# Optimization experiments

Hardware: AMD Instinct MI355X
Metric: run time of the kernel (lower is better)

The kernel has to match this reference:

```python
import jax, jax.numpy as jnp
import numpy as np

B = 16      # number of point clouds
N = 4096    # points per cloud (max after densify)
D = 3       # xyz


def setup_inputs() -> dict:
    key = jax.random.key(0)
    k1, k2 = jax.random.split(key)
    pred = jax.random.normal(k1, (B * N, D), dtype=jnp.float32)
    target = jax.random.normal(k2, (B * N, D), dtype=jnp.float32)
    # sorted segment ids, equal-sized clouds (faithful to to_dense_batch usage)
    batch = jnp.repeat(jnp.arange(B, dtype=jnp.int64), N)
    return {"pred": pred, "target": target, "batch": batch}


def to_dense_batch(x, batch, num_batches, max_n):
    # PyG to_dense_batch: scatter flat points into [B, max_n, D], zero-padded.
    ones = jnp.ones_like(batch)
    counts = jax.ops.segment_sum(ones, batch, num_segments=num_batches)
    offsets = jnp.concatenate([jnp.zeros((1,), batch.dtype), jnp.cumsum(counts)[:-1]])
    pos = jnp.arange(batch.shape[0], dtype=batch.dtype) - offsets[batch]
    dense = jnp.zeros((num_batches, max_n, x.shape[-1]), x.dtype)
    return dense.at[batch, pos].set(x)


def chamfer_distance(x, y):
    # squared-euclidean pairwise distances via the GEMM identity
    x2 = jnp.sum(x * x, axis=-1)                      # [B, N]
    y2 = jnp.sum(y * y, axis=-1)                      # [B, M]
    xy = jnp.einsum('bnd,bmd->bnm', x, y)             # [B, N, M]
    d = x2[:, :, None] + y2[:, None, :] - 2.0 * xy    # [B, N, M]
    cham_x = jnp.mean(jnp.min(d, axis=2), axis=1)     # mean over N of min over M
    cham_y = jnp.mean(jnp.min(d, axis=1), axis=1)     # mean over M of min over N
    # point_reduction='mean', batch_reduction='mean' (pytorch3d defaults)
    return jnp.mean(cham_x + cham_y)


def reference(pred, target, batch):
    x = to_dense_batch(pred, batch, B, N)
    y = to_dense_batch(target, batch, B, N)
    return chamfer_distance(x, y)
```

## Files before the change

### kernel.cpp

```cpp
#include <hip/hip_runtime.h>


namespace {

constexpr int kB = 16;
constexpr int kN = 4096;
constexpr int kPlane = kB * kN;
constexpr int kJS = 8;
constexpr int kJSL = kN / kJS;
constexpr float kScale = 1.0f / (float)(kB * kN);

typedef short bf16x8 __attribute__((ext_vector_type(8)));
typedef float f32x16 __attribute__((ext_vector_type(16)));
typedef unsigned short u16;

__device__ inline u16 bf16_rn(float f) {
  union { float f; unsigned u; } v; v.f = f;
  unsigned r = v.u + 0x7fffu + ((v.u >> 16) & 1u);
  return (u16)(r >> 16);
}
__device__ inline float bf16_f(u16 h) {
  union { unsigned u; float f; } v; v.u = (unsigned)h << 16;
  return v.f;
}
__device__ inline unsigned pk2(u16 lo, u16 hi) {
  return (unsigned)lo | ((unsigned)hi << 16);
}

__device__ inline float min3f(float a, float b, float c) {
  float d;
  asm("v_min3_f32 %0, %1, %2, %3" : "=v"(d) : "v"(a), "v"(b), "v"(c));
  return d;
}

__global__ void init_out(float* out) { out[0] = 0.0f; }

__global__ __launch_bounds__(256) void cd_mfma(
    const float* __restrict__ pred, const float* __restrict__ targ,
    float* __restrict__ colpart, float* __restrict__ rowpart,
    float* __restrict__ out) {
  __shared__ uint4 Blds4[kJSL * 2];
  __shared__ float clds[4 * kJSL];

  const int t = threadIdx.x;
  const int w = t >> 6, lane = t & 63;
  const int half = lane >> 5, l31 = lane & 31;
  const int chunk = blockIdx.x;
  const int cloud = blockIdx.y;
  const int slice = blockIdx.z;

  if ((t | chunk | cloud | slice) == 0) out[0] = 0.0f;

  const u16 one = 0x3F80;

  const int arow = cloud * kN + chunk * 128 + w * 32 + l31;
  union { uint4 u; bf16x8 v; } afu;
  {
    const float a = pred[3 * arow], c = pred[3 * arow + 1], d = pred[3 * arow + 2];
    const u16 ah = bf16_rn(a), ch = bf16_rn(c), dh = bf16_rn(d);
    const u16 al = bf16_rn(a - bf16_f(ah));
    const u16 cl = bf16_rn(c - bf16_f(ch));
    const u16 dl = bf16_rn(d - bf16_f(dh));
    const float s2 = fmaf(a, a, fmaf(c, c, d * d));
    const u16 s2h = bf16_rn(s2);
    const u16 s2l = bf16_rn(s2 - bf16_f(s2h));
    if (half == 0) {
      afu.u.x = pk2(ah, ch); afu.u.y = pk2(dh, al);
      afu.u.z = pk2(cl, dl); afu.u.w = pk2(ah, ch);
    } else {
      afu.u.x = pk2(dh, s2h); afu.u.y = pk2(s2l, one);
      afu.u.z = pk2(one, al); afu.u.w = pk2(cl, dl);
    }
  }
  const bf16x8 afrag = afu.v;

  {
    const float* tb = targ + (size_t)(cloud * kN + slice * kJSL) * 3;
    char* bl = (char*)Blds4;
    for (int pl = t; pl < kJSL; pl += 256) {
      const float a = tb[3 * pl], c = tb[3 * pl + 1], d = tb[3 * pl + 2];
      const u16 ah0 = bf16_rn(a), ch0 = bf16_rn(c), dh0 = bf16_rn(d);
      const u16 ah = bf16_rn(-2.0f * bf16_f(ah0));
      const u16 ch = bf16_rn(-2.0f * bf16_f(ch0));
      const u16 dh = bf16_rn(-2.0f * bf16_f(dh0));
      const u16 al = bf16_rn(-2.0f * bf16_f(bf16_rn(a - bf16_f(ah0))));
      const u16 cl = bf16_rn(-2.0f * bf16_f(bf16_rn(c - bf16_f(ch0))));
      const u16 dl = bf16_rn(-2.0f * bf16_f(bf16_rn(d - bf16_f(dh0))));
      const float s2 = fmaf(a, a, fmaf(c, c, d * d));
      const u16 s2h = bf16_rn(s2);
      const u16 s2l = bf16_rn(s2 - bf16_f(s2h));
      uint4 w0, w1;
      w0.x = pk2(ah, ch); w0.y = pk2(dh, ah); w0.z = pk2(ch, dh); w0.w = pk2(al, cl);
      w1.x = pk2(dl, one); w1.y = pk2(one, s2h); w1.z = pk2(s2l, al); w1.w = pk2(cl, dl);
      const int sw = (pl & 7) << 4;
      *reinterpret_cast<uint4*>(bl + ((pl * 32) ^ sw)) = w0;
      *reinterpret_cast<uint4*>(bl + ((pl * 32 + 16) ^ sw)) = w1;
    }
  }
  __syncthreads();

  f32x16 zacc;
#pragma unroll
  for (int r = 0; r < 16; ++r) zacc[r] = 0.0f;
  float rmin[16];
#pragma unroll
  for (int r = 0; r < 16; ++r) rmin[r] = 1e30f;

  constexpr int NT = kJSL / 64;
  const char* bl = (const char*)Blds4;
  int addr0 = (l31 * 32 + half * 16) ^ ((l31 & 7) << 4);
  for (int jt = 0; jt < NT; ++jt) {
    union { uint4 u; bf16x8 v; } B0, B1;
    B0.u = *reinterpret_cast<const uint4*>(bl + addr0);
    B1.u = *reinterpret_cast<const uint4*>(bl + addr0 + 1024);
    addr0 += 2048;
    const f32x16 s0 = __builtin_amdgcn_mfma_f32_32x32x16_bf16(afrag, B0.v, zacc, 0, 0, 0);
    const f32x16 s1 = __builtin_amdgcn_mfma_f32_32x32x16_bf16(afrag, B1.v, zacc, 0, 0, 0);
    float a0 = min3f(s0[0], s0[1], s0[2]);
    float a1 = min3f(s0[3], s0[4], s0[5]);
    float a2 = min3f(s0[6], s0[7], s0[8]);
    float a3 = min3f(s0[9], s0[10], s0[11]);
    float a4 = min3f(s0[12], s0[13], s0[14]);
    float cm0 = fminf(min3f(a0, a1, a2), min3f(a3, a4, s0[15]));
    float b0t = min3f(s1[0], s1[1], s1[2]);
    float b1t = min3f(s1[3], s1[4], s1[5]);
    float b2t = min3f(s1[6], s1[7], s1[8]);
    float b3t = min3f(s1[9], s1[10], s1[11]);
    float b4t = min3f(s1[12], s1[13], s1[14]);
    float cm1 = fminf(min3f(b0t, b1t, b2t), min3f(b3t, b4t, s1[15]));
#pragma unroll
    for (int r = 0; r < 16; ++r)
      asm("v_min3_f32 %0, %0, %1, %2" : "+v"(rmin[r]) : "v"(s0[r]), "v"(s1[r]));
    cm0 = fminf(cm0, __shfl_xor(cm0, 32, 64));
    cm1 = fminf(cm1, __shfl_xor(cm1, 32, 64));
    if (half == 0) {
      clds[w * kJSL + jt * 64 + l31] = cm0;
      clds[w * kJSL + jt * 64 + 32 + l31] = cm1;
    }
  }

#pragma unroll
  for (int st = 1; st < 32; st <<= 1) {
#pragma unroll
    for (int r = 0; r < 16; ++r)
      rmin[r] = fminf(rmin[r], __shfl_xor(rmin[r], st, 64));
  }
  if (l31 == 0) {
    float* rp = rowpart + ((size_t)slice * kB + cloud) * kN + chunk * 128 + w * 32;
#pragma unroll
    for (int r = 0; r < 16; ++r) {
      const int row = (r & 3) + 8 * (r >> 2) + 4 * half;
      rp[row] = rmin[r];
    }
  }

  __syncthreads();
  for (int j = t; j < kJSL; j += 256) {
    const float m = fminf(fminf(clds[j], clds[kJSL + j]),
                          fminf(clds[2 * kJSL + j], clds[3 * kJSL + j]));
    colpart[((size_t)cloud * 32 + chunk) * kN + slice * kJSL + j] = m;
  }
}

__global__ __launch_bounds__(256) void cd_reduce(
    const float* __restrict__ colpart, const float* __restrict__ rowpart,
    float* __restrict__ out) {
  const int u = blockIdx.x * 256 + threadIdx.x;
  const int cloud = u >> 12, p = u & (kN - 1);
  float rm = 1e30f;
#pragma unroll
  for (int s2 = 0; s2 < kJS; ++s2)
    rm = fminf(rm, rowpart[((size_t)s2 * kB + cloud) * kN + p]);
  const float* cp = colpart + (size_t)cloud * 32 * kN + p;
  float cm = 1e30f;
#pragma unroll 8
  for (int c = 0; c < 32; ++c) cm = fminf(cm, cp[(size_t)c * kN]);
  float s = rm + cm;
  for (int o = 32; o > 0; o >>= 1) s += __shfl_down(s, o, 64);
  __shared__ float wsum[4];
  const int lane = threadIdx.x & 63, wv = threadIdx.x >> 6;
  if (lane == 0) wsum[wv] = s;
  __syncthreads();
  if (threadIdx.x == 0)
    atomicAdd(out, (wsum[0] + wsum[1] + wsum[2] + wsum[3]) * kScale);
}

template <int KX>
__global__ __launch_bounds__(256) void chamfer_direct(
    const float* __restrict__ pred, const float* __restrict__ targ,
    float* __restrict__ out) {
  __shared__ float4 tA[128], tB[128];
  const int t = threadIdx.x;
  const int xb = blockIdx.x, b = blockIdx.y, dir = blockIdx.z;
  const float* __restrict__ X = dir ? targ : pred;
  const float* __restrict__ Y = dir ? pred : targ;
  float2 xx2[KX], xy2[KX], xz2[KX];
  float x2[KX], mn[KX];
  const int ibase = b * kN + xb * (256 * KX) + t;
#pragma unroll
  for (int k = 0; k < KX; ++k) {
    const int i = ibase + k * 256;
    const float a = X[3 * i], c = X[3 * i + 1], d = X[3 * i + 2];
    x2[k] = fmaf(a, a, fmaf(c, c, d * d));
    xx2[k] = make_float2(-2.0f * a, -2.0f * a);
    xy2[k] = make_float2(-2.0f * c, -2.0f * c);
    xz2[k] = make_float2(-2.0f * d, -2.0f * d);
    mn[k] = 1e30f;
  }
  for (int t0 = 0; t0 < kN; t0 += 256) {
    __syncthreads();
    if (t < 128) {
      const int j0 = 3 * (b * kN + t0 + 2 * t);
      const float a0 = Y[j0], c0 = Y[j0 + 1], d0 = Y[j0 + 2];
      const float a1 = Y[j0 + 3], c1 = Y[j0 + 4], d1 = Y[j0 + 5];
      tA[t] = make_float4(a0, a1, c0, c1);
      tB[t] = make_float4(d0, d1, fmaf(a0, a0, fmaf(c0, c0, d0 * d0)),
                          fmaf(a1, a1, fmaf(c1, c1, d1 * d1)));
    }
    __syncthreads();
    for (int jj = 0; jj < 128; ++jj) {
      const float4 qa = tA[jj], qb = tB[jj];
      const float2 qx = make_float2(qa.x, qa.y), qy = make_float2(qa.z, qa.w);
      const float2 qz = make_float2(qb.x, qb.y), qw = make_float2(qb.z, qb.w);
#pragma unroll
      for (int k = 0; k < KX; ++k) {
        float2 acc;
        asm("v_pk_fma_f32 %0, %1, %2, %3\n\t"
            "v_pk_fma_f32 %0, %4, %5, %0\n\t"
            "v_pk_fma_f32 %0, %6, %7, %0"
            : "=&v"(acc)
            : "v"(xz2[k]), "v"(qz), "v"(qw), "v"(xy2[k]), "v"(qy),
              "v"(xx2[k]), "v"(qx));
        asm("v_min3_f32 %0, %0, %1, %2" : "+v"(mn[k]) : "v"(acc.x), "v"(acc.y));
      }
    }
  }
  float s = 0.0f;
#pragma unroll
  for (int k = 0; k < KX; ++k) s += x2[k] + mn[k];
  for (int o = 32; o > 0; o >>= 1) s += __shfl_down(s, o, 64);
  __shared__ float wsum[4];
  const int lane = t & 63, wv = t >> 6;
  if (lane == 0) wsum[wv] = s;
  __syncthreads();
  if (t == 0)
    atomicAdd(out, (wsum[0] + wsum[1] + wsum[2] + wsum[3]) * kScale);
}

}

extern "C" void kernel_launch(void* const* d_in, const int* in_sizes, int n_in,
                              void* d_out, int out_size, void* d_ws,
                              size_t ws_size, hipStream_t stream) {
  const float* pred = (const float*)d_in[0];
  const float* targ = (const float*)d_in[1];
  float* out = (float*)d_out;

  const size_t needCol = (size_t)kB * 32 * kN * sizeof(float);
  const size_t needRow = (size_t)kJS * kPlane * sizeof(float);
  if (ws_size >= needCol + needRow) {
    float* colpart = (float*)d_ws;
    float* rowpart = (float*)((char*)d_ws + needCol);
    cd_mfma<<<dim3(32, kB, kJS), 256, 0, stream>>>(pred, targ, colpart,
                                                   rowpart, out);
    cd_reduce<<<dim3(kPlane / 256), 256, 0, stream>>>(colpart, rowpart, out);
  } else {
    init_out<<<dim3(1), dim3(1), 0, stream>>>(out);
    constexpr int KX = 8;
    dim3 grid(kN / (256 * KX), kB, 2);
    chamfer_direct<KX><<<grid, 256, 0, stream>>>(pred, targ, out);
  }
}
```

Measured before the change: 100.8 us.

## Fuse chamfer into one MFMA kernel computing both directions with row mins

The previous design computed the distance matrix once and extracted both row minima and column minima. Column minima were written to workspace partial buffers, and a second reduce kernel combined them. The new design runs the MFMA distance computation twice, once per direction (grid z=2). Each block streams the full other cloud through shared memory in 512-point stages and keeps only per-row minima reduced in registers, finishing with an atomic add. This removes the column-min shuffles and LDS writes, the workspace traffic and the reduce launch, but doubles MFMA work and adds per-stage syncs.

New measurement: 94.53 us. 6.2% less time.

```diff
diff --git a/kernel.cpp b/kernel.cpp
--- a/kernel.cpp
+++ b/kernel.cpp
@@ -5,9 +5,8 @@
 
 constexpr int kB = 16;
 constexpr int kN = 4096;
-constexpr int kPlane = kB * kN;
-constexpr int kJS = 8;
-constexpr int kJSL = kN / kJS;
+constexpr int kStage = 512;
+constexpr int kNS = kN / kStage;
 constexpr float kScale = 1.0f / (float)(kB * kN);
 
 typedef short bf16x8 __attribute__((ext_vector_type(8)));
@@ -27,36 +26,29 @@
   return (unsigned)lo | ((unsigned)hi << 16);
 }
 
-__device__ inline float min3f(float a, float b, float c) {
-  float d;
-  asm("v_min3_f32 %0, %1, %2, %3" : "=v"(d) : "v"(a), "v"(b), "v"(c));
-  return d;
-}
-
 __global__ void init_out(float* out) { out[0] = 0.0f; }
 
-__global__ __launch_bounds__(256) void cd_mfma(
+__global__ __launch_bounds__(256) void cd_fused(
     const float* __restrict__ pred, const float* __restrict__ targ,
-    float* __restrict__ colpart, float* __restrict__ rowpart,
     float* __restrict__ out) {
-  __shared__ uint4 Blds4[kJSL * 2];
-  __shared__ float clds[4 * kJSL];
+  __shared__ uint4 Blds4[kStage * 2];
+  __shared__ float wsum[4];
 
   const int t = threadIdx.x;
   const int w = t >> 6, lane = t & 63;
   const int half = lane >> 5, l31 = lane & 31;
   const int chunk = blockIdx.x;
   const int cloud = blockIdx.y;
-  const int slice = blockIdx.z;
-
-  if ((t | chunk | cloud | slice) == 0) out[0] = 0.0f;
+  const int dir = blockIdx.z;
+  const float* __restrict__ X = dir ? targ : pred;
+  const float* __restrict__ Y = dir ? pred : targ;
 
   const u16 one = 0x3F80;
 
   const int arow = cloud * kN + chunk * 128 + w * 32 + l31;
   union { uint4 u; bf16x8 v; } afu;
   {
-    const float a = pred[3 * arow], c = pred[3 * arow + 1], d = pred[3 * arow + 2];
+    const float a = X[3 * arow], c = X[3 * arow + 1], d = X[3 * arow + 2];
     const u16 ah = bf16_rn(a), ch = bf16_rn(c), dh = bf16_rn(d);
     const u16 al = bf16_rn(a - bf16_f(ah));
     const u16 cl = bf16_rn(c - bf16_f(ch));
@@ -74,31 +66,6 @@
   }
   const bf16x8 afrag = afu.v;
 
-  {
-    const float* tb = targ + (size_t)(cloud * kN + slice * kJSL) * 3;
-    char* bl = (char*)Blds4;
-    for (int pl = t; pl < kJSL; pl += 256) {
-      const float a = tb[3 * pl], c = tb[3 * pl + 1], d = tb[3 * pl + 2];
-      const u16 ah0 = bf16_rn(a), ch0 = bf16_rn(c), dh0 = bf16_rn(d);
-      const u16 ah = bf16_rn(-2.0f * bf16_f(ah0));
-      const u16 ch = bf16_rn(-2.0f * bf16_f(ch0));
-      const u16 dh = bf16_rn(-2.0f * bf16_f(dh0));
-      const u16 al = bf16_rn(-2.0f * bf16_f(bf16_rn(a - bf16_f(ah0))));
-      const u16 cl = bf16_rn(-2.0f * bf16_f(bf16_rn(c - bf16_f(ch0))));
-      const u16 dl = bf16_rn(-2.0f * bf16_f(bf16_rn(d - bf16_f(dh0))));
-      const float s2 = fmaf(a, a, fmaf(c, c, d * d));
-      const u16 s2h = bf16_rn(s2);
-      const u16 s2l = bf16_rn(s2 - bf16_f(s2h));
-      uint4 w0, w1;
-      w0.x = pk2(ah, ch); w0.y = pk2(dh, ah); w0.z = pk2(ch, dh); w0.w = pk2(al, cl);
-      w1.x = pk2(dl, one); w1.y = pk2(one, s2h); w1.z = pk2(s2l, al); w1.w = pk2(cl, dl);
-      const int sw = (pl & 7) << 4;
-      *reinterpret_cast<uint4*>(bl + ((pl * 32) ^ sw)) = w0;
-      *reinterpret_cast<uint4*>(bl + ((pl * 32 + 16) ^ sw)) = w1;
-    }
-  }
-  __syncthreads();
-
   f32x16 zacc;
 #pragma unroll
   for (int r = 0; r < 16; ++r) zacc[r] = 0.0f;
@@ -106,36 +73,54 @@
 #pragma unroll
   for (int r = 0; r < 16; ++r) rmin[r] = 1e30f;
 
-  constexpr int NT = kJSL / 64;
-  const char* bl = (const char*)Blds4;
-  int addr0 = (l31 * 32 + half * 16) ^ ((l31 & 7) << 4);
-  for (int jt = 0; jt < NT; ++jt) {
-    union { uint4 u; bf16x8 v; } B0, B1;
-    B0.u = *reinterpret_cast<const uint4*>(bl + addr0);
-    B1.u = *reinterpret_cast<const uint4*>(bl + addr0 + 1024);
-    addr0 += 2048;
-    const f32x16 s0 = __builtin_amdgcn_mfma_f32_32x32x16_bf16(afrag, B0.v, zacc, 0, 0, 0);
-    const f32x16 s1 = __builtin_amdgcn_mfma_f32_32x32x16_bf16(afrag, B1.v, zacc, 0, 0, 0);
-    float a0 = min3f(s0[0], s0[1], s0[2]);
-    float a1 = min3f(s0[3], s0[4], s0[5]);
-    float a2 = min3f(s0[6], s0[7], s0[8]);
-    float a3 = min3f(s0[9], s0[10], s0[11]);
-    float a4 = min3f(s0[12], s0[13], s0[14]);
-    float cm0 = fminf(min3f(a0, a1, a2), min3f(a3, a4, s0[15]));
-    float b0t = min3f(s1[0], s1[1], s1[2]);
-    float b1t = min3f(s1[3], s1[4], s1[5]);
-    float b2t = min3f(s1[6], s1[7], s1[8]);
-    float b3t = min3f(s1[9], s1[10], s1[11]);
-    float b4t = min3f(s1[12], s1[13], s1[14]);
-    float cm1 = fminf(min3f(b0t, b1t, b2t), min3f(b3t, b4t, s1[15]));
+  const float* yb = Y + (size_t)cloud * kN * 3;
+  const int raddr = (l31 * 32 + half * 16) ^ ((l31 & 7) << 4);
+
+  for (int st = 0; st < kNS; ++st) {
+    __syncthreads();
+    {
+      char* bl = (char*)Blds4;
+      for (int pl = t; pl < kStage; pl += 256) {
+        const int gp = st * kStage + pl;
+        const float a = yb[3 * gp], c = yb[3 * gp + 1], d = yb[3 * gp + 2];
+        const u16 ah0 = bf16_rn(a), ch0 = bf16_rn(c), dh0 = bf16_rn(d);
+        const u16 ah = bf16_rn(-2.0f * bf16_f(ah0));
+        const u16 ch = bf16_rn(-2.0f * bf16_f(ch0));
+        const u16 dh = bf16_rn(-2.0f * bf16_f(dh0));
+        const u16 al = bf16_rn(-2.0f * bf16_f(bf16_rn(a - bf16_f(ah0))));
+        const u16 cl = bf16_rn(-2.0f * bf16_f(bf16_rn(c - bf16_f(ch0))));
+        const u16 dl = bf16_rn(-2.0f * bf16_f(bf16_rn(d - bf16_f(dh0))));
+        const float s2 = fmaf(a, a, fmaf(c, c, d * d));
+        const u16 s2h = bf16_rn(s2);
+        const u16 s2l = bf16_rn(s2 - bf16_f(s2h));
+        uint4 w0, w1;
+        w0.x = pk2(ah, ch); w0.y = pk2(dh, ah);
+        w0.z = pk2(ch, dh); w0.w = pk2(al, cl);
+        w1.x = pk2(dl, one); w1.y = pk2(one, s2h);
+        w1.z = pk2(s2l, al); w1.w = pk2(cl, dl);
+        const int sw = (pl & 7) << 4;
+        *reinterpret_cast<uint4*>(bl + ((pl * 32) ^ sw)) = w0;
+        *reinterpret_cast<uint4*>(bl + ((pl * 32 + 16) ^ sw)) = w1;
+      }
+    }
+    __syncthreads();
+
+    const char* blc = (const char*)Blds4;
+    int addr0 = raddr;
 #pragma unroll
-    for (int r = 0; r < 16; ++r)
-      asm("v_min3_f32 %0, %0, %1, %2" : "+v"(rmin[r]) : "v"(s0[r]), "v"(s1[r]));
-    cm0 = fminf(cm0, __shfl_xor(cm0, 32, 64));
-    cm1 = fminf(cm1, __shfl_xor(cm1, 32, 64));
-    if (half == 0) {
-      clds[w * kJSL + jt * 64 + l31] = cm0;
-      clds[w * kJSL + jt * 64 + 32 + l31] = cm1;
+    for (int jt = 0; jt < kStage / 64; ++jt) {
+      union { uint4 u; bf16x8 v; } B0, B1;
+      B0.u = *reinterpret_cast<const uint4*>(blc + addr0);
+      B1.u = *reinterpret_cast<const uint4*>(blc + addr0 + 1024);
+      addr0 += 2048;
+      const f32x16 s0 =
+          __builtin_amdgcn_mfma_f32_32x32x16_bf16(afrag, B0.v, zacc, 0, 0, 0);
+      const f32x16 s1 =
+          __builtin_amdgcn_mfma_f32_32x32x16_bf16(afrag, B1.v, zacc, 0, 0, 0);
+#pragma unroll
+      for (int r = 0; r < 16; ++r)
+        asm("v_min3_f32 %0, %0, %1, %2"
+            : "+v"(rmin[r]) : "v"(s0[r]), "v"(s1[r]));
     }
   }
 
@@ -145,103 +130,12 @@
     for (int r = 0; r < 16; ++r)
       rmin[r] = fminf(rmin[r], __shfl_xor(rmin[r], st, 64));
   }
-  if (l31 == 0) {
-    float* rp = rowpart + ((size_t)slice * kB + cloud) * kN + chunk * 128 + w * 32;
-#pragma unroll
-    for (int r = 0; r < 16; ++r) {
-      const int row = (r & 3) + 8 * (r >> 2) + 4 * half;
-      rp[row] = rmin[r];
-    }
-  }
-
-  __syncthreads();
-  for (int j = t; j < kJSL; j += 256) {
-    const float m = fminf(fminf(clds[j], clds[kJSL + j]),
-                          fminf(clds[2 * kJSL + j], clds[3 * kJSL + j]));
-    colpart[((size_t)cloud * 32 + chunk) * kN + slice * kJSL + j] = m;
-  }
-}
-
-__global__ __launch_bounds__(256) void cd_reduce(
-    const float* __restrict__ colpart, const float* __restrict__ rowpart,
-    float* __restrict__ out) {
-  const int u = blockIdx.x * 256 + threadIdx.x;
-  const int cloud = u >> 12, p = u & (kN - 1);
-  float rm = 1e30f;
-#pragma unroll
-  for (int s2 = 0; s2 < kJS; ++s2)
-    rm = fminf(rm, rowpart[((size_t)s2 * kB + cloud) * kN + p]);
-  const float* cp = colpart + (size_t)cloud * 32 * kN + p;
-  float cm = 1e30f;
-#pragma unroll 8
-  for (int c = 0; c < 32; ++c) cm = fminf(cm, cp[(size_t)c * kN]);
-  float s = rm + cm;
-  for (int o = 32; o > 0; o >>= 1) s += __shfl_down(s, o, 64);
-  __shared__ float wsum[4];
-  const int lane = threadIdx.x & 63, wv = threadIdx.x >> 6;
-  if (lane == 0) wsum[wv] = s;
-  __syncthreads();
-  if (threadIdx.x == 0)
-    atomicAdd(out, (wsum[0] + wsum[1] + wsum[2] + wsum[3]) * kScale);
-}
-
-template <int KX>
-__global__ __launch_bounds__(256) void chamfer_direct(
-    const float* __restrict__ pred, const float* __restrict__ targ,
-    float* __restrict__ out) {
-  __shared__ float4 tA[128], tB[128];
-  const int t = threadIdx.x;
-  const int xb = blockIdx.x, b = blockIdx.y, dir = blockIdx.z;
-  const float* __restrict__ X = dir ? targ : pred;
-  const float* __restrict__ Y = dir ? pred : targ;
-  float2 xx2[KX], xy2[KX], xz2[KX];
-  float x2[KX], mn[KX];
-  const int ibase = b * kN + xb * (256 * KX) + t;
-#pragma unroll
-  for (int k = 0; k < KX; ++k) {
-    const int i = ibase + k * 256;
-    const float a = X[3 * i], c = X[3 * i + 1], d = X[3 * i + 2];
-    x2[k] = fmaf(a, a, fmaf(c, c, d * d));
-    xx2[k] = make_float2(-2.0f * a, -2.0f * a);
-    xy2[k] = make_float2(-2.0f * c, -2.0f * c);
-    xz2[k] = make_float2(-2.0f * d, -2.0f * d);
-    mn[k] = 1e30f;
-  }
-  for (int t0 = 0; t0 < kN; t0 += 256) {
-    __syncthreads();
-    if (t < 128) {
-      const int j0 = 3 * (b * kN + t0 + 2 * t);
-      const float a0 = Y[j0], c0 = Y[j0 + 1], d0 = Y[j0 + 2];
-      const float a1 = Y[j0 + 3], c1 = Y[j0 + 4], d1 = Y[j0 + 5];
-      tA[t] = make_float4(a0, a1, c0, c1);
-      tB[t] = make_float4(d0, d1, fmaf(a0, a0, fmaf(c0, c0, d0 * d0)),
-                          fmaf(a1, a1, fmaf(c1, c1, d1 * d1)));
-    }
-    __syncthreads();
-    for (int jj = 0; jj < 128; ++jj) {
-      const float4 qa = tA[jj], qb = tB[jj];
-      const float2 qx = make_float2(qa.x, qa.y), qy = make_float2(qa.z, qa.w);
-      const float2 qz = make_float2(qb.x, qb.y), qw = make_float2(qb.z, qb.w);
-#pragma unroll
-      for (int k = 0; k < KX; ++k) {
-        float2 acc;
-        asm("v_pk_fma_f32 %0, %1, %2, %3\n\t"
-            "v_pk_fma_f32 %0, %4, %5, %0\n\t"
-            "v_pk_fma_f32 %0, %6, %7, %0"
-            : "=&v"(acc)
-            : "v"(xz2[k]), "v"(qz), "v"(qw), "v"(xy2[k]), "v"(qy),
-              "v"(xx2[k]), "v"(qx));
-        asm("v_min3_f32 %0, %0, %1, %2" : "+v"(mn[k]) : "v"(acc.x), "v"(acc.y));
-      }
-    }
-  }
   float s = 0.0f;
 #pragma unroll
-  for (int k = 0; k < KX; ++k) s += x2[k] + mn[k];
-  for (int o = 32; o > 0; o >>= 1) s += __shfl_down(s, o, 64);
-  __shared__ float wsum[4];
-  const int lane = t & 63, wv = t >> 6;
-  if (lane == 0) wsum[wv] = s;
+  for (int r = 0; r < 16; ++r) s += rmin[r];
+  s = (l31 == 0) ? s : 0.0f;
+  s += __shfl_down(s, 32, 64);
+  if (lane == 0) wsum[w] = s;
   __syncthreads();
   if (t == 0)
     atomicAdd(out, (wsum[0] + wsum[1] + wsum[2] + wsum[3]) * kScale);
@@ -255,19 +149,8 @@
   const float* pred = (const float*)d_in[0];
   const float* targ = (const float*)d_in[1];
   float* out = (float*)d_out;
+  (void)d_ws; (void)ws_size;
 
-  const size_t needCol = (size_t)kB * 32 * kN * sizeof(float);
-  const size_t needRow = (size_t)kJS * kPlane * sizeof(float);
-  if (ws_size >= needCol + needRow) {
-    float* colpart = (float*)d_ws;
-    float* rowpart = (float*)((char*)d_ws + needCol);
-    cd_mfma<<<dim3(32, kB, kJS), 256, 0, stream>>>(pred, targ, colpart,
-                                                   rowpart, out);
-    cd_reduce<<<dim3(kPlane / 256), 256, 0, stream>>>(colpart, rowpart, out);
-  } else {
-    init_out<<<dim3(1), dim3(1), 0, stream>>>(out);
-    constexpr int KX = 8;
-    dim3 grid(kN / (256 * KX), kB, 2);
-    chamfer_direct<KX><<<grid, 256, 0, stream>>>(pred, targ, out);
-  }
+  init_out<<<dim3(1), dim3(1), 0, stream>>>(out);
+  cd_fused<<<dim3(32, kB, 2), 256, 0, stream>>>(pred, targ, out);
 }
```
